# Kernel optimization log

Measured on AMD Instinct MI355X. Metric: run time of the kernel, lower is better.

The kernel has to match this reference:

```python
import jax, jax.numpy as jnp
import numpy as np


def setup_inputs() -> dict:
    key = jax.random.key(0)
    k1, k2 = jax.random.split(key)
    N, F, E = 100000, 128, 600000
    x = jax.random.normal(k1, (N, F), dtype=jnp.float32)
    edge_index = jax.random.randint(k2, (2, E), 0, N, dtype=jnp.int64)
    return {"x": x, "edge_index": edge_index}


def reference(x, edge_index):
    # x: [N, F] node features; edge_index: [2, E]
    ei = edge_index.T  # [E, 2]
    N = x.shape[0]
    E = ei.shape[0]

    # Midpoint node insertion: mean of the two endpoint features per edge.
    mid = 0.5 * (x[ei[:, 0]] + x[ei[:, 1]])  # [E, F]
    new_x = jnp.concatenate([x, mid], axis=0)  # [N+E, F]

    # New node indices N .. N+E-1
    new_idx = jnp.arange(N, N + E)
    e1 = jnp.stack([ei[:, 0], new_idx], axis=1)  # src -> midpoint
    e2 = jnp.stack([new_idx, ei[:, 1]], axis=1)  # midpoint -> dst

    # Triangle edges among consecutive triples of new nodes (vectorized form
    # of the original Python loop: for i in range(N, N+E-2, 3)).
    T = -(-(E - 2) // 3) if E > 2 else 0  # ceil((E-2)/3) == number of loop iters
    i = N + 3 * jnp.arange(T)
    tri = jnp.stack([i, i + 1, i + 1, i + 2, i + 2, i], axis=1).reshape(-1, 2)  # [3T, 2]

    new_ei = jnp.concatenate([ei, e1, e2, tri], axis=0)  # [E + 2E + 3T, 2]
    return new_x, new_ei.T
```

## Files before the change

### kernel.cpp

```cpp
#include <hip/hip_runtime.h>


#define F 128
#define F4 32
#define BSHIFT 10
#define SLOTS 8192
#define SPB 256
#define CPB 32
#define BPB (SPB + CPB)
#define CHUNK 2048

typedef float f32x4 __attribute__((ext_vector_type(4)));
typedef unsigned long long u64;

__device__ __forceinline__ void nt_store4(f32x4 v, f32x4* p) {
    asm volatile("global_store_dwordx4 %0, %1, off sc0 sc1 nt"
                 :: "v"(p), "v"(v) : "memory");
}
__device__ __forceinline__ void nt_store1(float v, float* p) {
    asm volatile("global_store_dword %0, %1, off sc0 sc1 nt"
                 :: "v"(p), "v"(v) : "memory");
}

__global__ void init_kernel(int* __restrict__ cursor, int NB) {
    const int t = threadIdx.x;
    if (t < NB) cursor[t] = t * SLOTS;
}

__global__ __launch_bounds__(256) void scatter_kernel(
        const int* __restrict__ ei0, const int* __restrict__ ei1,
        int* __restrict__ cursor, u64* __restrict__ tup,
        float* __restrict__ r0, float* __restrict__ r1,
        int N, int E, int TT3, int NB) {
    __shared__ int lh[128];
    __shared__ int lbase[128];
    const int t = threadIdx.x;
    if (t < 128) lh[t] = 0;
    __syncthreads();
    const int base = blockIdx.x * CHUNK;
    int s[8], d[8], bk[8], rk[8];
#pragma unroll
    for (int i = 0; i < 8; ++i) {
        const int e = base + i * 256 + t;
        if (e < E) {
            s[i] = ei0[e];
            d[i] = ei1[e];
            bk[i] = s[i] >> BSHIFT;
            rk[i] = atomicAdd(&lh[bk[i]], 1);
            const float fs = (float)s[i], fd = (float)d[i], fm = (float)(N + e);
            nt_store1(fs, &r0[e]);
            nt_store1(fd, &r1[e]);
            nt_store1(fs, &r0[E + e]);
            nt_store1(fm, &r1[E + e]);
            nt_store1(fm, &r0[2 * E + e]);
            nt_store1(fd, &r1[2 * E + e]);
        } else {
            bk[i] = -1;
        }
        if (e < TT3) {
            const int tt = e / 3;
            const int k = e - 3 * tt;
            const int ii = N + 3 * tt;
            nt_store1((float)(ii + k), &r0[3 * E + e]);
            nt_store1((float)((k < 2) ? (ii + k + 1) : ii), &r1[3 * E + e]);
        }
    }
    __syncthreads();
    if (t < NB) {
        const int c = lh[t];
        lbase[t] = c ? atomicAdd(&cursor[t], c) : 0;
    }
    __syncthreads();
#pragma unroll
    for (int i = 0; i < 8; ++i) {
        if (bk[i] >= 0) {
            const int e = base + i * 256 + t;
            const int pos = lbase[bk[i]] + rk[i];
            if (pos < (bk[i] + 1) * SLOTS) {
                const u64 pk = (u64)(e | ((s[i] & 1023) << 20));
                tup[pos] = (pk << 32) | (unsigned)d[i];
            }
        }
    }
}

__global__ __launch_bounds__(256) void main_kernel(
        const f32x4* __restrict__ x4,
        const u64* __restrict__ tup, const int* __restrict__ cursor,
        f32x4* __restrict__ out4,
        int N, int NB, int MBlk) {
    const unsigned b = blockIdx.x;
    if (b >= (unsigned)MBlk) return;
    const int xcd = b & 7;
    const int seq = b >> 3;
    const int bucket = xcd + 8 * (seq / BPB);
    if (bucket >= NB) return;
    const int r = seq % BPB;
    const int lane = threadIdx.x & 31;
    const int g = threadIdx.x >> 5;

    if (r < SPB) {
        const int cnt = cursor[bucket] - bucket * SLOTS;
        const int si0 = r * 32 + g * 4;
        if (si0 >= cnt) return;
        const int p0 = bucket * SLOTS + si0;
        const int nbase = bucket << BSHIFT;
        const int nv = min(4, cnt - si0);

        u64 tv[4];
        f32x4 av[4], bv[4];
        int ev[4];
#pragma unroll
        for (int j = 0; j < 4; ++j)
            tv[j] = (j < nv) ? tup[p0 + j] : 0;
#pragma unroll
        for (int j = 0; j < 4; ++j) {
            const int dj = (int)(tv[j] & 0xffffffffu);
            const int pkj = (int)(tv[j] >> 32);
            const int sj = nbase | (pkj >> 20);
            ev[j] = pkj & 0xFFFFF;
            if (j < nv) {
                av[j] = x4[(size_t)sj * F4 + lane];
                bv[j] = x4[(size_t)dj * F4 + lane];
            }
        }
#pragma unroll
        for (int j = 0; j < 4; ++j) {
            if (j < nv)
                nt_store4(0.5f * (av[j] + bv[j]),
                          &out4[(size_t)(N + ev[j]) * F4 + lane]);
        }
    } else {
        const int cr = r - SPB;
        const long long row0 = ((long long)bucket << BSHIFT) + cr * 32 + g * 4;
        f32x4 v[4];
        const int nv = (int)min((long long)4, (long long)N - row0);
#pragma unroll
        for (int j = 0; j < 4; ++j)
            if (j < nv) v[j] = x4[(row0 + j) * F4 + lane];
#pragma unroll
        for (int j = 0; j < 4; ++j)
            if (j < nv) nt_store4(v[j], &out4[(row0 + j) * F4 + lane]);
    }
}

extern "C" void kernel_launch(void* const* d_in, const int* in_sizes, int n_in,
                              void* d_out, int out_size, void* d_ws, size_t ws_size,
                              hipStream_t stream) {
    const float* x = (const float*)d_in[0];
    const int* ei = (const int*)d_in[1];

    const int N = in_sizes[0] / F;
    const int E = in_sizes[1] / 2;
    const int T = (E > 2) ? (E - 2 + 2) / 3 : 0;
    const int M = 3 * E + 3 * T;

    const int* ei0 = ei;
    const int* ei1 = ei + E;

    float* out = (float*)d_out;
    float* r0 = out + (size_t)(N + E) * F;
    float* r1 = r0 + M;

    int* cursor = (int*)d_ws;
    u64* tup = (u64*)((char*)d_ws + 4096);

    const int NB = (N + (1 << BSHIFT) - 1) >> BSHIFT;
    const int NBpad = (NB + 7) & ~7;
    const int MBlk = NBpad * BPB;

    init_kernel<<<1, 128, 0, stream>>>(cursor, NB);
    scatter_kernel<<<(E + CHUNK - 1) / CHUNK, 256, 0, stream>>>(
        ei0, ei1, cursor, tup, r0, r1, N, E, 3 * T, NB);
    main_kernel<<<MBlk, 256, 0, stream>>>(
        (const f32x4*)x, tup, cursor, (f32x4*)out, N, NB, MBlk);
}
```

Baseline: 127.0 us.

## Move node-feature copy into scatter kernel and replace init kernel with memset

The straight copy of x into the output moves from the midpoint gather kernel into extra blocks of the scatter kernel, so it overlaps with edge bucketing and runs one kernel earlier. The init kernel is replaced by a hipMemsetAsync that zeroes the per-bucket cursors, and the cursors become relative offsets. The midpoint kernel now does only the gather-average work. Risk: the copy blocks now compete with the scatter blocks for bandwidth, and the memset may cost as much as the launch it replaces.

```diff
diff --git a/kernel.cpp b/kernel.cpp
--- a/kernel.cpp
+++ b/kernel.cpp
@@ -1,4 +1,5 @@
 #include <hip/hip_runtime.h>
+#include <string.h>
 
 
 #define F 128
@@ -6,8 +7,6 @@
 #define BSHIFT 10
 #define SLOTS 8192
 #define SPB 256
-#define CPB 32
-#define BPB (SPB + CPB)
 #define CHUNK 2048
 
 typedef float f32x4 __attribute__((ext_vector_type(4)));
@@ -22,16 +21,28 @@
                  :: "v"(p), "v"(v) : "memory");
 }
 
-__global__ void init_kernel(int* __restrict__ cursor, int NB) {
-    const int t = threadIdx.x;
-    if (t < NB) cursor[t] = t * SLOTS;
-}
-
-__global__ __launch_bounds__(256) void scatter_kernel(
+__global__ __launch_bounds__(256) void scatter_copy_kernel(
         const int* __restrict__ ei0, const int* __restrict__ ei1,
+        const f32x4* __restrict__ x4, f32x4* __restrict__ out4,
         int* __restrict__ cursor, u64* __restrict__ tup,
         float* __restrict__ r0, float* __restrict__ r1,
-        int N, int E, int TT3, int NB) {
+        int N, int E, int TT3, int NB, int SB) {
+    if (blockIdx.x >= (unsigned)SB) {
+        const unsigned cb = blockIdx.x - SB;
+        const int lane = threadIdx.x & 31;
+        const int g = threadIdx.x >> 5;
+        const long long row0 = (long long)cb * 32 + g * 4;
+        const int nv = (int)min((long long)4, (long long)N - row0);
+        f32x4 v[4];
+#pragma unroll
+        for (int j = 0; j < 4; ++j)
+            if (j < nv) v[j] = x4[(row0 + j) * F4 + lane];
+#pragma unroll
+        for (int j = 0; j < 4; ++j)
+            if (j < nv) nt_store4(v[j], &out4[(row0 + j) * F4 + lane]);
+        return;
+    }
+
     __shared__ int lh[128];
     __shared__ int lbase[128];
     const int t = threadIdx.x;
@@ -75,16 +86,16 @@
     for (int i = 0; i < 8; ++i) {
         if (bk[i] >= 0) {
             const int e = base + i * 256 + t;
-            const int pos = lbase[bk[i]] + rk[i];
-            if (pos < (bk[i] + 1) * SLOTS) {
+            const int off = lbase[bk[i]] + rk[i];
+            if (off < SLOTS) {
                 const u64 pk = (u64)(e | ((s[i] & 1023) << 20));
-                tup[pos] = (pk << 32) | (unsigned)d[i];
+                tup[(size_t)bk[i] * SLOTS + off] = (pk << 32) | (unsigned)d[i];
             }
         }
     }
 }
 
-__global__ __launch_bounds__(256) void main_kernel(
+__global__ __launch_bounds__(256) void midpoint_kernel(
         const f32x4* __restrict__ x4,
         const u64* __restrict__ tup, const int* __restrict__ cursor,
         f32x4* __restrict__ out4,
@@ -93,54 +104,41 @@
     if (b >= (unsigned)MBlk) return;
     const int xcd = b & 7;
     const int seq = b >> 3;
-    const int bucket = xcd + 8 * (seq / BPB);
+    const int bucket = xcd + 8 * (seq / SPB);
     if (bucket >= NB) return;
-    const int r = seq % BPB;
+    const int r = seq % SPB;
     const int lane = threadIdx.x & 31;
     const int g = threadIdx.x >> 5;
 
-    if (r < SPB) {
-        const int cnt = cursor[bucket] - bucket * SLOTS;
-        const int si0 = r * 32 + g * 4;
-        if (si0 >= cnt) return;
-        const int p0 = bucket * SLOTS + si0;
-        const int nbase = bucket << BSHIFT;
-        const int nv = min(4, cnt - si0);
+    const int cnt = min(cursor[bucket], SLOTS);
+    const int si0 = r * 32 + g * 4;
+    if (si0 >= cnt) return;
+    const size_t p0 = (size_t)bucket * SLOTS + si0;
+    const int nbase = bucket << BSHIFT;
+    const int nv = min(4, cnt - si0);
 
-        u64 tv[4];
-        f32x4 av[4], bv[4];
-        int ev[4];
+    u64 tv[4];
+    f32x4 av[4], bv[4];
+    int ev[4];
 #pragma unroll
-        for (int j = 0; j < 4; ++j)
-            tv[j] = (j < nv) ? tup[p0 + j] : 0;
+    for (int j = 0; j < 4; ++j)
+        tv[j] = (j < nv) ? tup[p0 + j] : 0;
 #pragma unroll
-        for (int j = 0; j < 4; ++j) {
-            const int dj = (int)(tv[j] & 0xffffffffu);
-            const int pkj = (int)(tv[j] >> 32);
-            const int sj = nbase | (pkj >> 20);
-            ev[j] = pkj & 0xFFFFF;
-            if (j < nv) {
-                av[j] = x4[(size_t)sj * F4 + lane];
-                bv[j] = x4[(size_t)dj * F4 + lane];
-            }
+    for (int j = 0; j < 4; ++j) {
+        const int dj = (int)(tv[j] & 0xffffffffu);
+        const int pkj = (int)(tv[j] >> 32);
+        const int sj = nbase | (pkj >> 20);
+        ev[j] = pkj & 0xFFFFF;
+        if (j < nv) {
+            av[j] = x4[(size_t)sj * F4 + lane];
+            bv[j] = x4[(size_t)dj * F4 + lane];
         }
+    }
 #pragma unroll
-        for (int j = 0; j < 4; ++j) {
-            if (j < nv)
-                nt_store4(0.5f * (av[j] + bv[j]),
-                          &out4[(size_t)(N + ev[j]) * F4 + lane]);
-        }
-    } else {
-        const int cr = r - SPB;
-        const long long row0 = ((long long)bucket << BSHIFT) + cr * 32 + g * 4;
-        f32x4 v[4];
-        const int nv = (int)min((long long)4, (long long)N - row0);
-#pragma unroll
-        for (int j = 0; j < 4; ++j)
-            if (j < nv) v[j] = x4[(row0 + j) * F4 + lane];
-#pragma unroll
-        for (int j = 0; j < 4; ++j)
-            if (j < nv) nt_store4(v[j], &out4[(row0 + j) * F4 + lane]);
+    for (int j = 0; j < 4; ++j) {
+        if (j < nv)
+            nt_store4(0.5f * (av[j] + bv[j]),
+                      &out4[(size_t)(N + ev[j]) * F4 + lane]);
     }
 }
 
@@ -167,11 +165,14 @@
 
     const int NB = (N + (1 << BSHIFT) - 1) >> BSHIFT;
     const int NBpad = (NB + 7) & ~7;
-    const int MBlk = NBpad * BPB;
+    const int SB = (E + CHUNK - 1) / CHUNK;
+    const int CB = (N + 31) / 32;
+    const int MBlk = NBpad * SPB;
 
-    init_kernel<<<1, 128, 0, stream>>>(cursor, NB);
-    scatter_kernel<<<(E + CHUNK - 1) / CHUNK, 256, 0, stream>>>(
-        ei0, ei1, cursor, tup, r0, r1, N, E, 3 * T, NB);
-    main_kernel<<<MBlk, 256, 0, stream>>>(
+    hipMemsetAsync(cursor, 0, NB * sizeof(int), stream);
+    scatter_copy_kernel<<<SB + CB, 256, 0, stream>>>(
+        ei0, ei1, (const f32x4*)x, (f32x4*)out, cursor, tup, r0, r1,
+        N, E, 3 * T, NB, SB);
+    midpoint_kernel<<<MBlk, 256, 0, stream>>>(
         (const f32x4*)x, tup, cursor, (f32x4*)out, N, NB, MBlk);
 }
```

Measured after the change: 131.8 us. 1.04x slower.
